# Kernel optimization log

Hardware: AMD Instinct MI355X
Metric: run time of the kernel (lower is better)

## Reference

```python
import jax, jax.numpy as jnp
import numpy as np

N, E = 50000, 400000
IN_DIM, OUT_DIM, EDGE_DIM, HEADS = 128, 32, 64, 8
N_REL = 512
NEG_SLOPE = 0.2  # GATv2 leaky_relu slope


def setup_inputs() -> dict:
    key = jax.random.key(0)
    ks = jax.random.split(key, 12)
    HC = HEADS * OUT_DIM
    return {
        "x": jax.random.normal(ks[0], (N, IN_DIM), jnp.float32),
        "edge_index": jax.random.randint(ks[1], (2, E), 0, N),
        "relations": jax.random.normal(ks[2], (N_REL, EDGE_DIM), jnp.float32),
        "relation_index": jax.random.randint(ks[3], (E,), 0, N_REL),
        "W_l": jax.random.normal(ks[4], (IN_DIM, HC), jnp.float32) / np.sqrt(IN_DIM),
        "b_l": jnp.zeros((HC,), jnp.float32),
        "W_r": jax.random.normal(ks[5], (IN_DIM, HC), jnp.float32) / np.sqrt(IN_DIM),
        "b_r": jnp.zeros((HC,), jnp.float32),
        "W_e": jax.random.normal(ks[6], (EDGE_DIM, HC), jnp.float32) / np.sqrt(EDGE_DIM),
        "att": jax.random.normal(ks[7], (HEADS, OUT_DIM), jnp.float32) / np.sqrt(OUT_DIM),
        "bias": jnp.zeros((OUT_DIM,), jnp.float32),
    }


def reference(x, edge_index, relations, relation_index, W_l, b_l, W_r, b_r, W_e, att, bias):
    H, C = HEADS, OUT_DIM
    src, dst = edge_index[0], edge_index[1]
    edge_attr = relations[relation_index]                       # [E, edge_dim]

    # add_self_loops with fill_value='mean': self-loop attr = mean of incoming edge_attr
    deg = jax.ops.segment_sum(jnp.ones((E,), x.dtype), dst, num_segments=N)
    attr_sum = jax.ops.segment_sum(edge_attr, dst, num_segments=N)
    self_attr = attr_sum / jnp.maximum(deg, 1.0)[:, None]        # [N, edge_dim]

    loop = jnp.arange(N)
    src_f = jnp.concatenate([src, loop])                         # [E+N]
    dst_f = jnp.concatenate([dst, loop])
    ea_f = jnp.concatenate([edge_attr, self_attr], axis=0)       # [E+N, edge_dim]

    x_l = (x @ W_l + b_l).reshape(N, H, C)
    x_r = (x @ W_r + b_r).reshape(N, H, C)
    e_emb = (ea_f @ W_e).reshape(-1, H, C)                       # [E+N, H, C]

    # GATv2 scoring: leaky_relu(x_l[src] + x_r[dst] + e_emb) . att
    m = x_l[src_f] + x_r[dst_f] + e_emb                          # [E+N, H, C]
    m = jnp.where(m >= 0, m, NEG_SLOPE * m)
    logits = jnp.einsum("ehc,hc->eh", m, att)                    # [E+N, H]

    # segment softmax over destination node
    lmax = jax.ops.segment_max(logits, dst_f, num_segments=N)    # [N, H]
    ex = jnp.exp(logits - lmax[dst_f])
    denom = jax.ops.segment_sum(ex, dst_f, num_segments=N)       # [N, H]
    alpha = ex / denom[dst_f]                                    # [E+N, H]

    # scatter-add aggregation of alpha-weighted source features
    msg = alpha[:, :, None] * x_l[src_f]                         # [E+N, H, C]
    out = jax.ops.segment_sum(msg, dst_f, num_segments=N)        # [N, H, C]
    out = out.mean(axis=1) + bias                                # concat=False -> head mean
    return (out, relations)
```

## Files before the change

kernel.cpp:

```cpp
#include <hip/hip_runtime.h>

#define N_NODES   50000
#define N_EDGES   400000
#define IN_DIM    128
#define OUT_DIM   32
#define EDGE_DIM  64
#define HEADS     8
#define HC        256
#define N_REL     512
#define NEG_SLOPE 0.2f
#define NB_SCAN   196
#define KT        64

template<int K>
__global__ __launch_bounds__(256) void k_gemm(
        const float* __restrict__ A, const float* __restrict__ W,
        const float* __restrict__ bias, float* __restrict__ C, int M) {
    __shared__ float As[64][KT + 4];
    __shared__ float Ws[KT][64];
    const int bid = blockIdx.x;
    const int mt = bid >> 2, ct = bid & 3;
    const int n0 = mt * 64;
    const int c0 = ct * 64;
    const int t  = threadIdx.x;
    const int tx = t & 15, ty = t >> 4;

    float acc[4][4];
    if (bias) {
        const float4 b4 = *(const float4*)(bias + c0 + tx * 4);
#pragma unroll
        for (int mi = 0; mi < 4; ++mi) {
            acc[mi][0] = b4.x; acc[mi][1] = b4.y;
            acc[mi][2] = b4.z; acc[mi][3] = b4.w;
        }
    } else {
#pragma unroll
        for (int mi = 0; mi < 4; ++mi)
#pragma unroll
            for (int ci = 0; ci < 4; ++ci) acc[mi][ci] = 0.f;
    }

    for (int kt = 0; kt < K; kt += KT) {
#pragma unroll
        for (int i = t * 4; i < 64 * KT; i += 1024) {
            const int node = i >> 6;
            const int kk   = i & 63;
            const int row  = n0 + node;
            float4 v = make_float4(0.f, 0.f, 0.f, 0.f);
            if (row < M) v = *(const float4*)(A + (size_t)row * K + kt + kk);
            *(float4*)&As[node][kk] = v;
        }
#pragma unroll
        for (int i = t * 4; i < KT * 64; i += 1024) {
            const int kk = i >> 6;
            const int c  = i & 63;
            *(float4*)&Ws[kk][c] =
                *(const float4*)(W + (size_t)(kt + kk) * HC + c0 + c);
        }
        __syncthreads();

#pragma unroll
        for (int k = 0; k < KT; k += 4) {
            const float4 a0 = *(const float4*)&As[ty * 4 + 0][k];
            const float4 a1 = *(const float4*)&As[ty * 4 + 1][k];
            const float4 a2 = *(const float4*)&As[ty * 4 + 2][k];
            const float4 a3 = *(const float4*)&As[ty * 4 + 3][k];
            const float4 w0 = *(const float4*)&Ws[k + 0][tx * 4];
            const float4 w1 = *(const float4*)&Ws[k + 1][tx * 4];
            const float4 w2 = *(const float4*)&Ws[k + 2][tx * 4];
            const float4 w3 = *(const float4*)&Ws[k + 3][tx * 4];
#define GSTEP(mi, AV)                                                          \
            acc[mi][0] = fmaf(AV.x, w0.x, fmaf(AV.y, w1.x,                     \
                         fmaf(AV.z, w2.x, fmaf(AV.w, w3.x, acc[mi][0]))));     \
            acc[mi][1] = fmaf(AV.x, w0.y, fmaf(AV.y, w1.y,                     \
                         fmaf(AV.z, w2.y, fmaf(AV.w, w3.y, acc[mi][1]))));     \
            acc[mi][2] = fmaf(AV.x, w0.z, fmaf(AV.y, w1.z,                     \
                         fmaf(AV.z, w2.z, fmaf(AV.w, w3.z, acc[mi][2]))));     \
            acc[mi][3] = fmaf(AV.x, w0.w, fmaf(AV.y, w1.w,                     \
                         fmaf(AV.z, w2.w, fmaf(AV.w, w3.w, acc[mi][3]))))
            GSTEP(0, a0); GSTEP(1, a1); GSTEP(2, a2); GSTEP(3, a3);
#undef GSTEP
        }
        __syncthreads();
    }

#pragma unroll
    for (int mi = 0; mi < 4; ++mi) {
        const int row = n0 + ty * 4 + mi;
        if (row < M) {
            float4 o;
            o.x = acc[mi][0]; o.y = acc[mi][1];
            o.z = acc[mi][2]; o.w = acc[mi][3];
            *(float4*)(C + (size_t)row * HC + c0 + tx * 4) = o;
        }
    }
}

__global__ void k_deg(const int* __restrict__ dst_arr, int* __restrict__ deg_i) {
    const int e = blockIdx.x * 256 + threadIdx.x;
    if (e < N_EDGES) atomicAdd(&deg_i[dst_arr[e]], 1);
}

__global__ void __launch_bounds__(256) k_scan_a(const int* __restrict__ deg_i,
                                                int* __restrict__ incl,
                                                int* __restrict__ partials) {
    __shared__ int s[256];
    const int i = blockIdx.x * 256 + threadIdx.x;
    const int v = (i < N_NODES) ? deg_i[i] : 0;
    s[threadIdx.x] = v;
    __syncthreads();
#pragma unroll
    for (int o = 1; o < 256; o <<= 1) {
        int t = s[threadIdx.x];
        if (threadIdx.x >= o) t += s[threadIdx.x - o];
        __syncthreads();
        s[threadIdx.x] = t;
        __syncthreads();
    }
    if (i < N_NODES) incl[i] = s[threadIdx.x];
    if (threadIdx.x == 255) partials[blockIdx.x] = s[255];
}

__global__ void __launch_bounds__(256) k_scan_b(int* __restrict__ partials) {
    __shared__ int s[256];
    const int v = (threadIdx.x < NB_SCAN) ? partials[threadIdx.x] : 0;
    s[threadIdx.x] = v;
    __syncthreads();
#pragma unroll
    for (int o = 1; o < 256; o <<= 1) {
        int t = s[threadIdx.x];
        if (threadIdx.x >= o) t += s[threadIdx.x - o];
        __syncthreads();
        s[threadIdx.x] = t;
        __syncthreads();
    }
    if (threadIdx.x < NB_SCAN) partials[threadIdx.x] = s[threadIdx.x] - v;
}

__global__ void __launch_bounds__(256) k_scan_c(const int* __restrict__ incl,
                                                const int* __restrict__ deg_i,
                                                const int* __restrict__ partials,
                                                int* __restrict__ row_ptr) {
    const int i = blockIdx.x * 256 + threadIdx.x;
    if (i < N_NODES) row_ptr[i] = incl[i] - deg_i[i] + partials[blockIdx.x];
    if (i == 0) row_ptr[N_NODES] = N_EDGES;
}

__global__ void k_fill(const int* __restrict__ src_arr,
                       const int* __restrict__ dst_arr,
                       const int* __restrict__ rel_idx,
                       const int* __restrict__ row_ptr,
                       int* __restrict__ cursor,
                       int2* __restrict__ csr) {
    const int e = blockIdx.x * 256 + threadIdx.x;
    if (e >= N_EDGES) return;
    const int d = dst_arr[e];
    const int pos = row_ptr[d] + atomicAdd(&cursor[d], 1);
    csr[pos] = make_int2(src_arr[e], rel_idx[e]);
}

__global__ void __launch_bounds__(256) k_selfattr(
        const int* __restrict__ row_ptr, const int2* __restrict__ csr,
        const float* __restrict__ relations, float* __restrict__ self_attr) {
    const int n = (blockIdx.x * 256 + threadIdx.x) >> 6;
    if (n >= N_NODES) return;
    const int lane = threadIdx.x & 63;
    const int beg = row_ptr[n], end = row_ptr[n + 1];
    float a = 0.f;
    for (int i = beg; i < end; ++i) {
        const int r = csr[i].y;
        a += relations[r * EDGE_DIM + lane];
    }
    const float dg = (float)max(end - beg, 1);
    self_attr[n * EDGE_DIM + lane] = a / dg;
}

__global__ void __launch_bounds__(256) k_agg(
        const int* __restrict__ row_ptr, const int2* __restrict__ csr,
        const float* __restrict__ x_l, const float* __restrict__ x_r,
        const float* __restrict__ rel_emb, const float* __restrict__ self_emb,
        const float* __restrict__ att, const float* __restrict__ bias,
        float* __restrict__ out) {
    const int n = (blockIdx.x * 256 + threadIdx.x) >> 6;
    if (n >= N_NODES) return;
    const int lane = threadIdx.x & 63;
    const int q = lane & 7;
    const int off = (lane >> 3) * OUT_DIM + q * 4;

    const float4 at = *(const float4*)(att + off);
    const float4 xr = *(const float4*)(x_r + (size_t)n * HC + off);

    const float4 xls = *(const float4*)(x_l + (size_t)n * HC + off);
    const float4 se  = *(const float4*)(self_emb + (size_t)n * HC + off);
    float m0 = xls.x + xr.x + se.x; m0 = m0 >= 0.f ? m0 : NEG_SLOPE * m0;
    float m1 = xls.y + xr.y + se.y; m1 = m1 >= 0.f ? m1 : NEG_SLOPE * m1;
    float m2 = xls.z + xr.z + se.z; m2 = m2 >= 0.f ? m2 : NEG_SLOPE * m2;
    float m3 = xls.w + xr.w + se.w; m3 = m3 >= 0.f ? m3 : NEG_SLOPE * m3;
    float p = at.x * m0 + at.y * m1 + at.z * m2 + at.w * m3;
    p += __shfl_xor(p, 1);
    p += __shfl_xor(p, 2);
    p += __shfl_xor(p, 4);
    float ex = __expf(p);
    float den = ex;
    float4 acc;
    acc.x = ex * xls.x; acc.y = ex * xls.y; acc.z = ex * xls.z; acc.w = ex * xls.w;

    const int beg = row_ptr[n], end = row_ptr[n + 1];
    for (int i = beg; i < end; ++i) {
        const int2 sr = csr[i];
        const float4 xl = *(const float4*)(x_l + (size_t)sr.x * HC + off);
        const float4 ev = *(const float4*)(rel_emb + (size_t)sr.y * HC + off);
        float a0 = xl.x + xr.x + ev.x; a0 = a0 >= 0.f ? a0 : NEG_SLOPE * a0;
        float a1 = xl.y + xr.y + ev.y; a1 = a1 >= 0.f ? a1 : NEG_SLOPE * a1;
        float a2 = xl.z + xr.z + ev.z; a2 = a2 >= 0.f ? a2 : NEG_SLOPE * a2;
        float a3 = xl.w + xr.w + ev.w; a3 = a3 >= 0.f ? a3 : NEG_SLOPE * a3;
        float pp = at.x * a0 + at.y * a1 + at.z * a2 + at.w * a3;
        pp += __shfl_xor(pp, 1);
        pp += __shfl_xor(pp, 2);
        pp += __shfl_xor(pp, 4);
        const float e2 = __expf(pp);
        den += e2;
        acc.x = fmaf(e2, xl.x, acc.x);
        acc.y = fmaf(e2, xl.y, acc.y);
        acc.z = fmaf(e2, xl.z, acc.z);
        acc.w = fmaf(e2, xl.w, acc.w);
    }

    const float inv = 1.f / den;
    float4 v;
    v.x = acc.x * inv; v.y = acc.y * inv; v.z = acc.z * inv; v.w = acc.w * inv;
    v.x += __shfl_xor(v.x, 8);  v.y += __shfl_xor(v.y, 8);
    v.z += __shfl_xor(v.z, 8);  v.w += __shfl_xor(v.w, 8);
    v.x += __shfl_xor(v.x, 16); v.y += __shfl_xor(v.y, 16);
    v.z += __shfl_xor(v.z, 16); v.w += __shfl_xor(v.w, 16);
    v.x += __shfl_xor(v.x, 32); v.y += __shfl_xor(v.y, 32);
    v.z += __shfl_xor(v.z, 32); v.w += __shfl_xor(v.w, 32);
    if (lane < 8) {
        const float4 bs = *(const float4*)(bias + q * 4);
        float4 o;
        o.x = v.x * 0.125f + bs.x;
        o.y = v.y * 0.125f + bs.y;
        o.z = v.z * 0.125f + bs.z;
        o.w = v.w * 0.125f + bs.w;
        *(float4*)(out + (size_t)n * OUT_DIM + q * 4) = o;
    }
}

__global__ void k_copy_rel(const float* __restrict__ relations,
                           float* __restrict__ out_tail) {
    const int i = blockIdx.x * 256 + threadIdx.x;
    if (i < N_REL * EDGE_DIM) out_tail[i] = relations[i];
}

extern "C" void kernel_launch(void* const* d_in, const int* in_sizes, int n_in,
                              void* d_out, int out_size, void* d_ws, size_t ws_size,
                              hipStream_t stream) {
    const float* x         = (const float*)d_in[0];
    const int*   edge_idx  = (const int*)d_in[1];
    const float* relations = (const float*)d_in[2];
    const int*   rel_idx   = (const int*)d_in[3];
    const float* W_l       = (const float*)d_in[4];
    const float* b_l       = (const float*)d_in[5];
    const float* W_r       = (const float*)d_in[6];
    const float* b_r       = (const float*)d_in[7];
    const float* W_e       = (const float*)d_in[8];
    const float* att       = (const float*)d_in[9];
    const float* bias      = (const float*)d_in[10];

    const int* src_arr = edge_idx;
    const int* dst_arr = edge_idx + N_EDGES;

    float* out      = (float*)d_out;
    float* out_tail = out + N_NODES * OUT_DIM;

    float* ws        = (float*)d_ws;
    float* x_l       = ws;
    float* x_r       = x_l + (size_t)N_NODES * HC;
    float* self_emb  = x_r + (size_t)N_NODES * HC;
    float* rel_emb   = self_emb + (size_t)N_NODES * HC;
    float* self_attr = rel_emb + (size_t)N_REL * HC;
    int*   ibase     = (int*)(self_attr + (size_t)N_NODES * EDGE_DIM);
    int2*  csr       = (int2*)ibase;
    int*   row_ptr   = ibase + 2 * N_EDGES;
    int*   incl      = row_ptr + N_NODES + 4;
    int*   deg_i     = incl + N_NODES;
    int*   cursor    = deg_i + N_NODES;
    int*   partials  = cursor + N_NODES;

    hipMemsetAsync(deg_i, 0, 2 * N_NODES * sizeof(int), stream);

    k_deg<<<(N_EDGES + 255) / 256, 256, 0, stream>>>(dst_arr, deg_i);
    k_scan_a<<<NB_SCAN, 256, 0, stream>>>(deg_i, incl, partials);
    k_scan_b<<<1, 256, 0, stream>>>(partials);
    k_scan_c<<<NB_SCAN, 256, 0, stream>>>(incl, deg_i, partials, row_ptr);
    k_fill<<<(N_EDGES + 255) / 256, 256, 0, stream>>>(
        src_arr, dst_arr, rel_idx, row_ptr, cursor, csr);

    const int mt_nodes = (N_NODES + 63) / 64;
    const int mt_rel   = (N_REL + 63) / 64;
    k_gemm<128><<<mt_nodes * 4, 256, 0, stream>>>(x, W_l, b_l, x_l, N_NODES);
    k_gemm<128><<<mt_nodes * 4, 256, 0, stream>>>(x, W_r, b_r, x_r, N_NODES);
    k_gemm<64><<<mt_rel * 4, 256, 0, stream>>>(relations, W_e, nullptr,
                                               rel_emb, N_REL);

    k_selfattr<<<(N_NODES * 64 + 255) / 256, 256, 0, stream>>>(
        row_ptr, csr, relations, self_attr);
    k_gemm<64><<<mt_nodes * 4, 256, 0, stream>>>(self_attr, W_e, nullptr,
                                                 self_emb, N_NODES);

    k_agg<<<(N_NODES * 64 + 255) / 256, 256, 0, stream>>>(
        row_ptr, csr, x_l, x_r, rel_emb, self_emb, att, bias, out);

    k_copy_rel<<<(N_REL * EDGE_DIM + 255) / 256, 256, 0, stream>>>(
        relations, out_tail);
}
```

Measured before the change: 448.8 us.

## Fuse x_l/x_r GEMMs into one dual-weight kernel with register prefetch

The two projections of x (W_l and W_r) now run in a single GEMM launch that loads each A tile once and accumulates into two sets of accumulators. Global loads for the next K tile are prefetched into registers while the current tile is computed, and launch bounds request three blocks per CU. This removes one launch and halves the reads of x, at the cost of more registers and shared memory per block, which may reduce occupancy.

```diff
diff --git a/kernel.cpp b/kernel.cpp
--- a/kernel.cpp
+++ b/kernel.cpp
@@ -12,12 +12,15 @@
 #define NB_SCAN   196
 #define KT        64
 
-template<int K>
-__global__ __launch_bounds__(256) void k_gemm(
-        const float* __restrict__ A, const float* __restrict__ W,
-        const float* __restrict__ bias, float* __restrict__ C, int M) {
+template<int K, bool DUAL>
+__global__ __launch_bounds__(256, 3) void k_gemm(
+        const float* __restrict__ A,
+        const float* __restrict__ W1, const float* __restrict__ b1,
+        const float* __restrict__ W2, const float* __restrict__ b2,
+        float* __restrict__ C1, float* __restrict__ C2, int M) {
     __shared__ float As[64][KT + 4];
-    __shared__ float Ws[KT][64];
+    __shared__ float W1s[KT][64];
+    __shared__ float W2s[DUAL ? KT : 1][64];
     const int bid = blockIdx.x;
     const int mt = bid >> 2, ct = bid & 3;
     const int n0 = mt * 64;
@@ -25,60 +28,103 @@
     const int t  = threadIdx.x;
     const int tx = t & 15, ty = t >> 4;
 
-    float acc[4][4];
-    if (bias) {
-        const float4 b4 = *(const float4*)(bias + c0 + tx * 4);
+    float acc1[4][4], acc2[4][4];
+    {
+        float4 b14 = make_float4(0.f, 0.f, 0.f, 0.f);
+        float4 b24 = make_float4(0.f, 0.f, 0.f, 0.f);
+        if (b1) b14 = *(const float4*)(b1 + c0 + tx * 4);
+        if (DUAL && b2) b24 = *(const float4*)(b2 + c0 + tx * 4);
 #pragma unroll
         for (int mi = 0; mi < 4; ++mi) {
-            acc[mi][0] = b4.x; acc[mi][1] = b4.y;
-            acc[mi][2] = b4.z; acc[mi][3] = b4.w;
-        }
-    } else {
-#pragma unroll
-        for (int mi = 0; mi < 4; ++mi)
-#pragma unroll
-            for (int ci = 0; ci < 4; ++ci) acc[mi][ci] = 0.f;
+            acc1[mi][0] = b14.x; acc1[mi][1] = b14.y;
+            acc1[mi][2] = b14.z; acc1[mi][3] = b14.w;
+            acc2[mi][0] = b24.x; acc2[mi][1] = b24.y;
+            acc2[mi][2] = b24.z; acc2[mi][3] = b24.w;
+        }
+    }
+
+    float4 ra[4], rw1[4], rw2[4];
+#pragma unroll
+    for (int j = 0; j < 4; ++j) {
+        const int i   = t + j * 256;
+        const int row = i >> 4;
+        const int cc  = (i & 15) * 4;
+        ra[j] = make_float4(0.f, 0.f, 0.f, 0.f);
+        if (n0 + row < M)
+            ra[j] = *(const float4*)(A + (size_t)(n0 + row) * K + cc);
+        rw1[j] = *(const float4*)(W1 + (size_t)row * HC + c0 + cc);
+        if (DUAL)
+            rw2[j] = *(const float4*)(W2 + (size_t)row * HC + c0 + cc);
     }
 
     for (int kt = 0; kt < K; kt += KT) {
 #pragma unroll
-        for (int i = t * 4; i < 64 * KT; i += 1024) {
-            const int node = i >> 6;
-            const int kk   = i & 63;
-            const int row  = n0 + node;
-            float4 v = make_float4(0.f, 0.f, 0.f, 0.f);
-            if (row < M) v = *(const float4*)(A + (size_t)row * K + kt + kk);
-            *(float4*)&As[node][kk] = v;
-        }
-#pragma unroll
-        for (int i = t * 4; i < KT * 64; i += 1024) {
-            const int kk = i >> 6;
-            const int c  = i & 63;
-            *(float4*)&Ws[kk][c] =
-                *(const float4*)(W + (size_t)(kt + kk) * HC + c0 + c);
-        }
-        __syncthreads();
-
-#pragma unroll
+        for (int j = 0; j < 4; ++j) {
+            const int i   = t + j * 256;
+            const int row = i >> 4;
+            const int cc  = (i & 15) * 4;
+            *(float4*)&As[row][cc]  = ra[j];
+            *(float4*)&W1s[row][cc] = rw1[j];
+            if (DUAL) *(float4*)&W2s[row][cc] = rw2[j];
+        }
+        __syncthreads();
+
+        if (kt + KT < K) {
+#pragma unroll
+            for (int j = 0; j < 4; ++j) {
+                const int i   = t + j * 256;
+                const int row = i >> 4;
+                const int cc  = (i & 15) * 4;
+                ra[j] = make_float4(0.f, 0.f, 0.f, 0.f);
+                if (n0 + row < M)
+                    ra[j] = *(const float4*)(A + (size_t)(n0 + row) * K +
+                                             kt + KT + cc);
+                rw1[j] = *(const float4*)(W1 + (size_t)(kt + KT + row) * HC +
+                                          c0 + cc);
+                if (DUAL)
+                    rw2[j] = *(const float4*)(W2 + (size_t)(kt + KT + row) * HC +
+                                              c0 + cc);
+            }
+        }
+
+#pragma unroll 2
         for (int k = 0; k < KT; k += 4) {
             const float4 a0 = *(const float4*)&As[ty * 4 + 0][k];
             const float4 a1 = *(const float4*)&As[ty * 4 + 1][k];
             const float4 a2 = *(const float4*)&As[ty * 4 + 2][k];
             const float4 a3 = *(const float4*)&As[ty * 4 + 3][k];
-            const float4 w0 = *(const float4*)&Ws[k + 0][tx * 4];
-            const float4 w1 = *(const float4*)&Ws[k + 1][tx * 4];
-            const float4 w2 = *(const float4*)&Ws[k + 2][tx * 4];
-            const float4 w3 = *(const float4*)&Ws[k + 3][tx * 4];
-#define GSTEP(mi, AV)                                                          \
-            acc[mi][0] = fmaf(AV.x, w0.x, fmaf(AV.y, w1.x,                     \
-                         fmaf(AV.z, w2.x, fmaf(AV.w, w3.x, acc[mi][0]))));     \
-            acc[mi][1] = fmaf(AV.x, w0.y, fmaf(AV.y, w1.y,                     \
-                         fmaf(AV.z, w2.y, fmaf(AV.w, w3.y, acc[mi][1]))));     \
-            acc[mi][2] = fmaf(AV.x, w0.z, fmaf(AV.y, w1.z,                     \
-                         fmaf(AV.z, w2.z, fmaf(AV.w, w3.z, acc[mi][2]))));     \
-            acc[mi][3] = fmaf(AV.x, w0.w, fmaf(AV.y, w1.w,                     \
-                         fmaf(AV.z, w2.w, fmaf(AV.w, w3.w, acc[mi][3]))))
-            GSTEP(0, a0); GSTEP(1, a1); GSTEP(2, a2); GSTEP(3, a3);
+            const float4 u0 = *(const float4*)&W1s[k + 0][tx * 4];
+            const float4 u1 = *(const float4*)&W1s[k + 1][tx * 4];
+            const float4 u2 = *(const float4*)&W1s[k + 2][tx * 4];
+            const float4 u3 = *(const float4*)&W1s[k + 3][tx * 4];
+#define GSTEP(ACC, mi, AV)                                                     \
+            ACC[mi][0] = fmaf(AV.x, u0.x, fmaf(AV.y, u1.x,                     \
+                         fmaf(AV.z, u2.x, fmaf(AV.w, u3.x, ACC[mi][0]))));     \
+            ACC[mi][1] = fmaf(AV.x, u0.y, fmaf(AV.y, u1.y,                     \
+                         fmaf(AV.z, u2.y, fmaf(AV.w, u3.y, ACC[mi][1]))));     \
+            ACC[mi][2] = fmaf(AV.x, u0.z, fmaf(AV.y, u1.z,                     \
+                         fmaf(AV.z, u2.z, fmaf(AV.w, u3.z, ACC[mi][2]))));     \
+            ACC[mi][3] = fmaf(AV.x, u0.w, fmaf(AV.y, u1.w,                     \
+                         fmaf(AV.z, u2.w, fmaf(AV.w, u3.w, ACC[mi][3]))))
+            GSTEP(acc1, 0, a0); GSTEP(acc1, 1, a1);
+            GSTEP(acc1, 2, a2); GSTEP(acc1, 3, a3);
+            if (DUAL) {
+                const float4 v0 = *(const float4*)&W2s[k + 0][tx * 4];
+                const float4 v1 = *(const float4*)&W2s[k + 1][tx * 4];
+                const float4 v2 = *(const float4*)&W2s[k + 2][tx * 4];
+                const float4 v3 = *(const float4*)&W2s[k + 3][tx * 4];
+#define GSTEP2(mi, AV)                                                         \
+            acc2[mi][0] = fmaf(AV.x, v0.x, fmaf(AV.y, v1.x,                    \
+                          fmaf(AV.z, v2.x, fmaf(AV.w, v3.x, acc2[mi][0]))));   \
+            acc2[mi][1] = fmaf(AV.x, v0.y, fmaf(AV.y, v1.y,                    \
+                          fmaf(AV.z, v2.y, fmaf(AV.w, v3.y, acc2[mi][1]))));   \
+            acc2[mi][2] = fmaf(AV.x, v0.z, fmaf(AV.y, v1.z,                    \
+                          fmaf(AV.z, v2.z, fmaf(AV.w, v3.z, acc2[mi][2]))));   \
+            acc2[mi][3] = fmaf(AV.x, v0.w, fmaf(AV.y, v1.w,                    \
+                          fmaf(AV.z, v2.w, fmaf(AV.w, v3.w, acc2[mi][3]))))
+                GSTEP2(0, a0); GSTEP2(1, a1); GSTEP2(2, a2); GSTEP2(3, a3);
+#undef GSTEP2
+            }
 #undef GSTEP
         }
         __syncthreads();
@@ -88,10 +134,16 @@
     for (int mi = 0; mi < 4; ++mi) {
         const int row = n0 + ty * 4 + mi;
         if (row < M) {
-            float4 o;
-            o.x = acc[mi][0]; o.y = acc[mi][1];
-            o.z = acc[mi][2]; o.w = acc[mi][3];
-            *(float4*)(C + (size_t)row * HC + c0 + tx * 4) = o;
+            float4 o1;
+            o1.x = acc1[mi][0]; o1.y = acc1[mi][1];
+            o1.z = acc1[mi][2]; o1.w = acc1[mi][3];
+            *(float4*)(C1 + (size_t)row * HC + c0 + tx * 4) = o1;
+            if (DUAL) {
+                float4 o2;
+                o2.x = acc2[mi][0]; o2.y = acc2[mi][1];
+                o2.z = acc2[mi][2]; o2.w = acc2[mi][3];
+                *(float4*)(C2 + (size_t)row * HC + c0 + tx * 4) = o2;
+            }
         }
     }
 }
@@ -298,15 +350,15 @@
 
     const int mt_nodes = (N_NODES + 63) / 64;
     const int mt_rel   = (N_REL + 63) / 64;
-    k_gemm<128><<<mt_nodes * 4, 256, 0, stream>>>(x, W_l, b_l, x_l, N_NODES);
-    k_gemm<128><<<mt_nodes * 4, 256, 0, stream>>>(x, W_r, b_r, x_r, N_NODES);
-    k_gemm<64><<<mt_rel * 4, 256, 0, stream>>>(relations, W_e, nullptr,
-                                               rel_emb, N_REL);
+    k_gemm<128, true><<<mt_nodes * 4, 256, 0, stream>>>(
+        x, W_l, b_l, W_r, b_r, x_l, x_r, N_NODES);
+    k_gemm<64, false><<<mt_rel * 4, 256, 0, stream>>>(
+        relations, W_e, nullptr, nullptr, nullptr, rel_emb, nullptr, N_REL);
 
     k_selfattr<<<(N_NODES * 64 + 255) / 256, 256, 0, stream>>>(
         row_ptr, csr, relations, self_attr);
-    k_gemm<64><<<mt_nodes * 4, 256, 0, stream>>>(self_attr, W_e, nullptr,
-                                                 self_emb, N_NODES);
+    k_gemm<64, false><<<mt_nodes * 4, 256, 0, stream>>>(
+        self_attr, W_e, nullptr, nullptr, nullptr, self_emb, nullptr, N_NODES);
 
     k_agg<<<(N_NODES * 64 + 255) / 256, 256, 0, stream>>>(
         row_ptr, csr, x_l, x_r, rel_emb, self_emb, att, bias, out);
```

Measured after the change: 400.8 us. 10.7% less time.
